# Kernel optimization log

Hardware: AMD Instinct MI355X
Metric: run time of the kernel (lower is better)

The kernel has to match this reference:

```python
import jax, jax.numpy as jnp
import numpy as np

B, N, M, H = 32, 1024, 256, 128


def setup_inputs() -> dict:
    key = jax.random.key(0)
    kA, kh, kW1, kW2 = jax.random.split(key, 4)
    A = jax.random.uniform(kA, (B, N, N), dtype=jnp.float32)
    h = jax.random.normal(kh, (B, N, M), dtype=jnp.float32)
    # torch Linear default init scale ~ 1/sqrt(fan_in)
    W1 = jax.random.normal(kW1, (M, H), dtype=jnp.float32) / np.sqrt(M)
    b1 = jnp.zeros((H,), dtype=jnp.float32)
    W2 = jax.random.normal(kW2, (H, M), dtype=jnp.float32) / np.sqrt(H)
    b2 = jnp.zeros((M,), dtype=jnp.float32)
    return {"A": A, "h": h, "W1": W1, "b1": b1, "W2": W2, "b2": b2}


def reference(A, h, W1, b1, W2, b2):
    # k = bmm(A, h) / 3 : [B,N,M]
    k = jnp.einsum('bij,bjm->bim', A, h) / 3.0
    # eta_g: Linear -> ReLU -> Linear
    k = jax.nn.relu(k @ W1 + b1) @ W2 + b2
    # A_mask = max over last dim of A, keepdims -> [B,N,1]
    A_mask = jnp.max(A, axis=-1, keepdims=True)
    # gated combine: k*mask + h*(mask-1)*(-1) == k*mask + h*(1-mask)
    return k * A_mask + h * (1.0 - A_mask)
```

## Files before the change

### kernel.cpp

```cpp
#include <hip/hip_runtime.h>

typedef __attribute__((ext_vector_type(8))) short bf16x8;
typedef __attribute__((ext_vector_type(4))) float f32x4;
typedef __attribute__((ext_vector_type(8))) unsigned short u16x8;

#define BB 32
#define NN 1024
#define MM 256
#define HH 128

__device__ __forceinline__ unsigned short f2bf(float f) {
  union { float f; unsigned int u; } c; c.f = f;
  unsigned int u = c.u + 0x7fffu + ((c.u >> 16) & 1u);
  return (unsigned short)(u >> 16);
}
__device__ __forceinline__ unsigned int cvtpk(float lo, float hi) {
  unsigned int r;
  asm("v_cvt_pk_bf16_f32 %0, %1, %2" : "=v"(r) : "v"(lo), "v"(hi));
  return r;
}
__device__ __forceinline__ float4 gload_f4(const float* p) {
  float4 r;
  asm volatile("global_load_dwordx4 %0, %1, off" : "=v"(r) : "v"(p));
  return r;
}
typedef __attribute__((address_space(3))) unsigned int as3_u32;
typedef const __attribute__((address_space(1))) unsigned int as1_u32;
__device__ __forceinline__ void gl_lds16(const void* g, void* l) {
  __builtin_amdgcn_global_load_lds((as1_u32*)g, (as3_u32*)l, 16, 0, 0);
}

__global__ __launch_bounds__(256)
void k_prep(const float* __restrict__ hg, unsigned short* __restrict__ hTg,
            const float* __restrict__ W1, const float* __restrict__ W2,
            unsigned short* __restrict__ W1T, unsigned short* __restrict__ W2T) {
  int bid = blockIdx.x;
  if (bid < BB * 64) {
    __shared__ unsigned short tile[64][65];
    int b = bid >> 6;
    int t = bid & 63;
    int k0 = (t >> 2) << 6;
    int m0 = (t & 3) << 6;
    int tt = threadIdx.x;
    {
      int r = tt >> 2;
      int cg = (tt & 3) << 4;
      const float* src = hg + (((size_t)b * NN + k0 + r) * MM + m0 + cg);
#pragma unroll
      for (int i = 0; i < 4; ++i) {
        float4 v = reinterpret_cast<const float4*>(src)[i];
        tile[r][cg + i * 4 + 0] = f2bf(v.x);
        tile[r][cg + i * 4 + 1] = f2bf(v.y);
        tile[r][cg + i * 4 + 2] = f2bf(v.z);
        tile[r][cg + i * 4 + 3] = f2bf(v.w);
      }
    }
    __syncthreads();
    {
      int mr = tt >> 2;
      int kc = (tt & 3) << 4;
      alignas(16) unsigned short tmp[16];
#pragma unroll
      for (int i = 0; i < 16; ++i) tmp[i] = tile[kc + i][mr];
      unsigned short* dst = hTg + (((size_t)b * MM + m0 + mr) * NN + k0 + kc);
      *reinterpret_cast<u16x8*>(dst)     = *reinterpret_cast<u16x8*>(tmp);
      *reinterpret_cast<u16x8*>(dst + 8) = *reinterpret_cast<u16x8*>(tmp + 8);
    }
  } else {
    int idx = (bid - BB * 64) * 256 + threadIdx.x;
    if (idx < MM * HH) {
      int hc = idx >> 8;
      int m  = idx & 255;
      W1T[idx] = f2bf(W1[m * HH + hc]);
    } else {
      int j = idx - MM * HH;
      int m  = j >> 7;
      int hd = j & 127;
      W2T[j] = f2bf(W2[hd * MM + m]);
    }
  }
}

#define HB0 0
#define HB1 32768
#define ABUF 65536
#define KLD 0
#define CLD 32768

#define PIPE_BARRIER() do { \
  asm volatile("s_waitcnt lgkmcnt(0)" ::: "memory"); \
  __builtin_amdgcn_s_barrier(); \
  asm volatile("" ::: "memory"); } while (0)

#define VMWAIT0() do { \
  asm volatile("s_waitcnt vmcnt(0)" ::: "memory"); \
  __builtin_amdgcn_sched_barrier(0); } while (0)

__global__ __launch_bounds__(512)
void k_fused(const float* __restrict__ Ag, const float* __restrict__ hg,
             const unsigned short* __restrict__ hTg,
             const unsigned short* __restrict__ W1Tg,
             const unsigned short* __restrict__ W2Tg,
             const float* __restrict__ b1g, const float* __restrict__ b2g,
             float* __restrict__ outg) {
  __shared__ __align__(16) char smem[73728];
  __shared__ float smax[64];

  const int tid  = threadIdx.x;
  const int lane = tid & 63;
  const int wid  = tid >> 6;
  const int wr   = wid >> 2;
  const int wc   = wid & 3;
  const int l15  = lane & 15;
  const int lg   = lane >> 4;

  const int bid = blockIdx.x;
  const int b   = bid & 31;
  const int r0  = (bid >> 5) << 6;

  const float* Ab = Ag + ((size_t)b * NN + r0) * NN;
  const unsigned short* hTb = hTg + (size_t)b * MM * NN;

  const int arow0 = tid >> 4;
  const int akc   = tid & 15;
  const float* apA0 = Ab + (size_t)arow0        * NN + (akc << 2);
  const float* apA1 = Ab + (size_t)(32 + arow0) * NN + (akc << 2);

  const unsigned short* baseH[4];
#pragma unroll
  for (int i = 0; i < 4; ++i) {
    int c = i * 512 + tid;
    int col = c >> 3, cic = c & 7;
    baseH[i] = hTb + (size_t)col * NN + ((cic ^ (col & 7)) << 3);
  }
  const int ldsW = wid << 10;

#define STAGE_H(K0, HB)                                                     \
  do {                                                                      \
    _Pragma("unroll")                                                       \
    for (int i = 0; i < 4; ++i)                                             \
      gl_lds16(baseH[i] + (K0), smem + (HB) + ldsW + i * 8192);             \
  } while (0)

  float4 rA0, rA1;
#define ISSUE_A(K0)                                                         \
  do {                                                                      \
    rA0 = gload_f4(apA0 + (K0));                                            \
    rA1 = gload_f4(apA1 + (K0));                                            \
  } while (0)

  float pm0 = -1e30f, pm1 = -1e30f;
#define CVTWR()                                                             \
  do {                                                                      \
    pm0 = fmaxf(pm0, fmaxf(fmaxf(rA0.x, rA0.y), fmaxf(rA0.z, rA0.w)));      \
    pm1 = fmaxf(pm1, fmaxf(fmaxf(rA1.x, rA1.y), fmaxf(rA1.z, rA1.w)));      \
    uint2 q0 = make_uint2(cvtpk(rA0.x, rA0.y), cvtpk(rA0.z, rA0.w));        \
    uint2 q1 = make_uint2(cvtpk(rA1.x, rA1.y), cvtpk(rA1.z, rA1.w));        \
    *reinterpret_cast<uint2*>(smem + ABUF + (arow0)      * 128 +            \
                              ((akc << 3) ^ ((arow0 & 7) << 4))) = q0;      \
    *reinterpret_cast<uint2*>(smem + ABUF + (32 + arow0) * 128 +            \
                              ((akc << 3) ^ ((arow0 & 7) << 4))) = q1;      \
  } while (0)

  f32x4 acc[2][4];
#pragma unroll
  for (int m = 0; m < 2; ++m)
#pragma unroll
    for (int n = 0; n < 4; ++n) acc[m][n] = f32x4{0.f, 0.f, 0.f, 0.f};

#define CONSUME(HB)                                                         \
  do {                                                                      \
    _Pragma("unroll")                                                       \
    for (int kk = 0; kk < 2; ++kk) {                                        \
      const int kb = (kk * 32 + (lg << 3)) * 2;                             \
      bf16x8 af[2], bh[4];                                                  \
      _Pragma("unroll")                                                     \
      for (int m = 0; m < 2; ++m) {                                         \
        int row = (wr << 5) + (m << 4) + l15;                               \
        af[m] = *reinterpret_cast<const bf16x8*>(                           \
            smem + ABUF + row * 128 + (kb ^ ((row & 7) << 4)));             \
      }                                                                     \
      _Pragma("unroll")                                                     \
      for (int n = 0; n < 4; ++n) {                                         \
        int col = (wc << 6) + (n << 4) + l15;                               \
        bh[n] = *reinterpret_cast<const bf16x8*>(                           \
            smem + (HB) + col * 128 + (kb ^ ((col & 7) << 4)));             \
      }                                                                     \
      _Pragma("unroll")                                                     \
      for (int m = 0; m < 2; ++m)                                           \
        _Pragma("unroll")                                                   \
        for (int n = 0; n < 4; ++n)                                         \
          acc[m][n] = __builtin_amdgcn_mfma_f32_16x16x32_bf16(af[m], bh[n], \
                                                              acc[m][n], 0, 0, 0); \
    }                                                                       \
  } while (0)

  STAGE_H(0, HB0);
  ISSUE_A(0);
  VMWAIT0();
  CVTWR();
  PIPE_BARRIER();

#pragma unroll
  for (int t = 0; t < 16; ++t) {
    if (t < 15) {
      STAGE_H((t + 1) * 64, (t & 1) ? HB0 : HB1);
      ISSUE_A((t + 1) * 64);
    }
    CONSUME((t & 1) ? HB1 : HB0);
    __builtin_amdgcn_s_barrier();
    if (t < 15) {
      VMWAIT0();
      CVTWR();
      PIPE_BARRIER();
    }
  }

  {
    float v0 = pm0, v1 = pm1;
#pragma unroll
    for (int s = 1; s < 16; s <<= 1) {
      v0 = fmaxf(v0, __shfl_xor(v0, s));
      v1 = fmaxf(v1, __shfl_xor(v1, s));
    }
    if ((tid & 15) == 0) {
      smax[arow0]      = v0;
      smax[32 + arow0] = v1;
    }
  }
  __syncthreads();

  {
    const float inv3 = 1.0f / 3.0f;
#pragma unroll
    for (int m = 0; m < 2; ++m)
#pragma unroll
      for (int n = 0; n < 4; ++n) {
        int col = (wc << 6) + (n << 4) + l15;
#pragma unroll
        for (int j = 0; j < 4; ++j) {
          int row = (wr << 5) + (m << 4) + (lg << 2) + j;
          *reinterpret_cast<unsigned short*>(smem + KLD + row * 512 +
                                             ((col * 2) ^ ((row & 7) << 4))) =
              f2bf(acc[m][n][j] * inv3);
        }
      }
  }
  __syncthreads();

  f32x4 acc1[2][2];
#pragma unroll
  for (int m = 0; m < 2; ++m)
#pragma unroll
    for (int n = 0; n < 2; ++n) acc1[m][n] = f32x4{0.f, 0.f, 0.f, 0.f};
  const int wcol1 = wc << 5;
#pragma unroll
  for (int kq = 0; kq < 8; ++kq) {
    bf16x8 af[2], bw[2];
#pragma unroll
    for (int m = 0; m < 2; ++m) {
      int row = (wr << 5) + (m << 4) + l15;
      af[m] = *reinterpret_cast<const bf16x8*>(smem + KLD + row * 512 +
              (((kq * 32 + (lg << 3)) * 2) ^ ((row & 7) << 4)));
    }
#pragma unroll
    for (int n = 0; n < 2; ++n) {
      int col = wcol1 + (n << 4) + l15;
      bw[n] = *reinterpret_cast<const bf16x8*>(W1Tg + (size_t)col * 256 +
                                               kq * 32 + (lg << 3));
    }
#pragma unroll
    for (int m = 0; m < 2; ++m)
#pragma unroll
      for (int n = 0; n < 2; ++n)
        acc1[m][n] = __builtin_amdgcn_mfma_f32_16x16x32_bf16(af[m], bw[n], acc1[m][n], 0, 0, 0);
  }
  __syncthreads();

  {
#pragma unroll
    for (int n = 0; n < 2; ++n) {
      int col = wcol1 + (n << 4) + l15;
      float bias = b1g[col];
#pragma unroll
      for (int m = 0; m < 2; ++m)
#pragma unroll
        for (int j = 0; j < 4; ++j) {
          int row = (wr << 5) + (m << 4) + (lg << 2) + j;
          float v = fmaxf(acc1[m][n][j] + bias, 0.f);
          *reinterpret_cast<unsigned short*>(smem + CLD + row * 256 +
                                             ((col * 2) ^ ((row & 7) << 4))) = f2bf(v);
        }
    }
  }
  __syncthreads();

  f32x4 acc2[2][4];
#pragma unroll
  for (int m = 0; m < 2; ++m)
#pragma unroll
    for (int n = 0; n < 4; ++n) acc2[m][n] = f32x4{0.f, 0.f, 0.f, 0.f};
#pragma unroll
  for (int kq = 0; kq < 4; ++kq) {
    bf16x8 af[2], bw[4];
#pragma unroll
    for (int m = 0; m < 2; ++m) {
      int row = (wr << 5) + (m << 4) + l15;
      af[m] = *reinterpret_cast<const bf16x8*>(smem + CLD + row * 256 +
              (((kq * 32 + (lg << 3)) * 2) ^ ((row & 7) << 4)));
    }
#pragma unroll
    for (int n = 0; n < 4; ++n) {
      int col = (wc << 6) + (n << 4) + l15;
      bw[n] = *reinterpret_cast<const bf16x8*>(W2Tg + (size_t)col * 128 +
                                               kq * 32 + (lg << 3));
    }
#pragma unroll
    for (int m = 0; m < 2; ++m)
#pragma unroll
      for (int n = 0; n < 4; ++n)
        acc2[m][n] = __builtin_amdgcn_mfma_f32_16x16x32_bf16(af[m], bw[n], acc2[m][n], 0, 0, 0);
  }

  {
#pragma unroll
    for (int n = 0; n < 4; ++n) {
      int col = (wc << 6) + (n << 4) + l15;
      float b2v = b2g[col];
#pragma unroll
      for (int m = 0; m < 2; ++m)
#pragma unroll
        for (int j = 0; j < 4; ++j) {
          int row = (wr << 5) + (m << 4) + (lg << 2) + j;
          float kv = acc2[m][n][j] + b2v;
          float mask = smax[row];
          size_t gidx = ((size_t)b * NN + r0 + row) * MM + col;
          float hv = hg[gidx];
          outg[gidx] = kv * mask + hv * (1.f - mask);
        }
    }
  }
#undef CONSUME
#undef CVTWR
#undef ISSUE_A
#undef STAGE_H
}

extern "C" void kernel_launch(void* const* d_in, const int* in_sizes, int n_in,
                              void* d_out, int out_size, void* d_ws, size_t ws_size,
                              hipStream_t stream) {
  (void)in_sizes; (void)n_in; (void)out_size; (void)ws_size;
  const float* A  = (const float*)d_in[0];
  const float* h  = (const float*)d_in[1];
  const float* W1 = (const float*)d_in[2];
  const float* b1 = (const float*)d_in[3];
  const float* W2 = (const float*)d_in[4];
  const float* b2 = (const float*)d_in[5];
  float* out = (float*)d_out;

  unsigned short* hT  = (unsigned short*)d_ws;
  unsigned short* W1T = (unsigned short*)((char*)d_ws + (size_t)BB * MM * NN * 2);
  unsigned short* W2T = W1T + MM * HH;

  k_prep<<<BB * 64 + 256, 256, 0, stream>>>(h, hT, W1, W2, W1T, W2T);
  k_fused<<<BB * 16, 512, 0, stream>>>(A, h, hT, W1T, W2T, b1, b2, out);
}
```

Baseline: 58.29 us.

## Double-buffer the A tile in LDS and drop the mid-loop barrier

Adds a second LDS buffer for the bf16-converted A tile. The next tile's convert and write now go into the other buffer while the current one is consumed, which makes the barrier after each consume step unnecessary. A loads are now issued before the H direct-to-LDS loads, and a partial vmcnt wait lets the A conversion start before the H loads finish. LDS use grows from 72 KB to 80 KB and smax now lives inside the shared buffer, which may affect occupancy.

```diff
diff --git a/kernel.cpp b/kernel.cpp
--- a/kernel.cpp
+++ b/kernel.cpp
@@ -83,17 +83,18 @@
 
 #define HB0 0
 #define HB1 32768
-#define ABUF 65536
+#define AB0 65536
+#define AB1 73728
 #define KLD 0
 #define CLD 32768
+#define SMAXOFF 65536
 
 #define PIPE_BARRIER() do { \
   asm volatile("s_waitcnt lgkmcnt(0)" ::: "memory"); \
   __builtin_amdgcn_s_barrier(); \
   asm volatile("" ::: "memory"); } while (0)
 
-#define VMWAIT0() do { \
-  asm volatile("s_waitcnt vmcnt(0)" ::: "memory"); \
+#define VMW(N) do { asm volatile("s_waitcnt vmcnt(" #N ")" ::: "memory"); \
   __builtin_amdgcn_sched_barrier(0); } while (0)
 
 __global__ __launch_bounds__(512)
@@ -103,8 +104,8 @@
              const unsigned short* __restrict__ W2Tg,
              const float* __restrict__ b1g, const float* __restrict__ b2g,
              float* __restrict__ outg) {
-  __shared__ __align__(16) char smem[73728];
-  __shared__ float smax[64];
+  __shared__ __align__(16) char smem[81920];
+  float* smax = reinterpret_cast<float*>(smem + SMAXOFF);
 
   const int tid  = threadIdx.x;
   const int lane = tid & 63;
@@ -150,15 +151,15 @@
   } while (0)
 
   float pm0 = -1e30f, pm1 = -1e30f;
-#define CVTWR()                                                             \
+#define CVTWR(AB)                                                           \
   do {                                                                      \
     pm0 = fmaxf(pm0, fmaxf(fmaxf(rA0.x, rA0.y), fmaxf(rA0.z, rA0.w)));      \
     pm1 = fmaxf(pm1, fmaxf(fmaxf(rA1.x, rA1.y), fmaxf(rA1.z, rA1.w)));      \
     uint2 q0 = make_uint2(cvtpk(rA0.x, rA0.y), cvtpk(rA0.z, rA0.w));        \
     uint2 q1 = make_uint2(cvtpk(rA1.x, rA1.y), cvtpk(rA1.z, rA1.w));        \
-    *reinterpret_cast<uint2*>(smem + ABUF + (arow0)      * 128 +            \
+    *reinterpret_cast<uint2*>(smem + (AB) + (arow0)      * 128 +            \
                               ((akc << 3) ^ ((arow0 & 7) << 4))) = q0;      \
-    *reinterpret_cast<uint2*>(smem + ABUF + (32 + arow0) * 128 +            \
+    *reinterpret_cast<uint2*>(smem + (AB) + (32 + arow0) * 128 +            \
                               ((akc << 3) ^ ((arow0 & 7) << 4))) = q1;      \
   } while (0)
 
@@ -168,7 +169,7 @@
 #pragma unroll
     for (int n = 0; n < 4; ++n) acc[m][n] = f32x4{0.f, 0.f, 0.f, 0.f};
 
-#define CONSUME(HB)                                                         \
+#define CONSUME(AB, HB)                                                     \
   do {                                                                      \
     _Pragma("unroll")                                                       \
     for (int kk = 0; kk < 2; ++kk) {                                        \
@@ -178,7 +179,7 @@
       for (int m = 0; m < 2; ++m) {                                         \
         int row = (wr << 5) + (m << 4) + l15;                               \
         af[m] = *reinterpret_cast<const bf16x8*>(                           \
-            smem + ABUF + row * 128 + (kb ^ ((row & 7) << 4)));             \
+            smem + (AB) + row * 128 + (kb ^ ((row & 7) << 4)));             \
       }                                                                     \
       _Pragma("unroll")                                                     \
       for (int n = 0; n < 4; ++n) {                                         \
@@ -195,23 +196,24 @@
     }                                                                       \
   } while (0)
 
+  ISSUE_A(0);
   STAGE_H(0, HB0);
-  ISSUE_A(0);
-  VMWAIT0();
-  CVTWR();
+  VMW(4);
+  CVTWR(AB0);
+  VMW(0);
   PIPE_BARRIER();
 
 #pragma unroll
   for (int t = 0; t < 16; ++t) {
     if (t < 15) {
+      ISSUE_A((t + 1) * 64);
       STAGE_H((t + 1) * 64, (t & 1) ? HB0 : HB1);
-      ISSUE_A((t + 1) * 64);
-    }
-    CONSUME((t & 1) ? HB1 : HB0);
-    __builtin_amdgcn_s_barrier();
+    }
+    CONSUME((t & 1) ? AB1 : AB0, (t & 1) ? HB1 : HB0);
     if (t < 15) {
-      VMWAIT0();
-      CVTWR();
+      VMW(4);
+      CVTWR((t & 1) ? AB0 : AB1);
+      VMW(0);
       PIPE_BARRIER();
     }
   }
```

Result: no change. 58.01 us (-0.5%).
